# Kernel optimization log

Measured on AMD Instinct MI355X. Metric: run time of the kernel, lower is better.

## Reference

```python
import jax, jax.numpy as jnp
import numpy as np

B, S, D, H = 2, 2048, 1024, 16
DEPTH = D // H  # 64


def setup_inputs() -> dict:
    key = jax.random.key(0)
    ks = jax.random.split(key, 12)
    sc = 0.02
    q = jax.random.normal(ks[0], (B, S, D), jnp.float32)
    k = jax.random.normal(ks[1], (B, S, D), jnp.float32)
    v = jax.random.normal(ks[2], (B, S, D), jnp.float32)
    mask = jax.random.randint(ks[3], (1, 1, S, S), 0, 2, jnp.int32)
    Wq = jax.random.normal(ks[4], (D, D), jnp.float32) * sc
    bq = jnp.zeros((D,), jnp.float32)
    Wk = jax.random.normal(ks[5], (D, D), jnp.float32) * sc
    bk = jnp.zeros((D,), jnp.float32)
    Wv = jax.random.normal(ks[6], (D, DEPTH), jnp.float32) * sc
    bv = jnp.zeros((DEPTH,), jnp.float32)
    Wo = jax.random.normal(ks[7], (DEPTH, D), jnp.float32) * sc
    bo = jnp.zeros((D,), jnp.float32)
    return {"q": q, "k": k, "v": v, "mask": mask,
            "Wq": Wq, "bq": bq, "Wk": Wk, "bk": bk,
            "Wv": Wv, "bv": bv, "Wo": Wo, "bo": bo}


def reference(q, k, v, mask, Wq, bq, Wk, bk, Wv, bv, Wo, bo):
    # project and split heads: [B,S,D] -> [B,H,S,depth]
    qh = (q @ Wq + bq).reshape(B, S, H, DEPTH).transpose(0, 2, 1, 3)
    kh = (k @ Wk + bk).reshape(B, S, H, DEPTH).transpose(0, 2, 1, 3)
    vp = v @ Wv + bv  # [B,S,depth], shared across heads (no per-head split)
    scale = 1.0 / jnp.sqrt(jnp.asarray(DEPTH, jnp.float32))
    logits = jnp.einsum("bhqd,bhkd->bhqk", qh, kh) * scale
    logits = logits + mask.astype(logits.dtype) * (-1e9)
    attn = jax.nn.softmax(logits, axis=-1)  # [B,H,Sq,Sk]
    attn_mean = jnp.mean(attn, axis=1)      # [B,Sq,Sk]
    # mean over heads of (attn_h @ v) == mean(attn) @ v since V is shared
    # (dropout is identity at inference)
    ctx = jnp.einsum("bqk,bkd->bqd", attn_mean, vp)  # [B,S,depth]
    out = ctx @ Wo + bo  # [B,S,D]
    return out, attn_mean
```

## Files before the change

### kernel.cpp

```cpp
#include <hip/hip_runtime.h>
#include <hip/hip_bf16.h>

#define BB 2
#define SS 2048
#define DD 1024
#define HH 16
#define DP 64

typedef __bf16 bf16x8 __attribute__((ext_vector_type(8)));
typedef float f32x4 __attribute__((ext_vector_type(4)));

__device__ __forceinline__ unsigned short f2bf(float f) {
  unsigned u = __float_as_uint(f);
  unsigned r = u + 0x7FFFu + ((u >> 16) & 1u);
  return (unsigned short)(r >> 16);
}

__device__ __forceinline__ bf16x8 load8(const unsigned short* p) {
  return __builtin_bit_cast(bf16x8, *(const uint4*)p);
}

__device__ __forceinline__ f32x4 mfma16(bf16x8 a, bf16x8 b, f32x4 c) {
  return __builtin_amdgcn_mfma_f32_16x16x32_bf16(a, b, c, 0, 0, 0);
}

__global__ __launch_bounds__(256) void imha_prep(
    const float* __restrict__ Wq, const float* __restrict__ Wk,
    const float* __restrict__ Wo, const float* __restrict__ Wv,
    const int* __restrict__ mask,
    unsigned short* __restrict__ wqt, unsigned short* __restrict__ wkt,
    unsigned short* __restrict__ wot, unsigned short* __restrict__ wvt,
    unsigned* __restrict__ mb) {
  const int bx = blockIdx.x, t = threadIdx.x;
  if (bx < 2048) {
    const float* src = (bx < 1024) ? Wq : Wk;
    unsigned short* dst = (bx < 1024) ? wqt : wkt;
    const int tile = bx & 1023;
    const int ty = tile >> 5, tx = tile & 31;
    __shared__ float T[32][33];
    const int r = t >> 3, c4 = (t & 7) * 4;
    const float4 v = *(const float4*)&src[(ty * 32 + r) * 1024 + tx * 32 + c4];
    T[r][c4 + 0] = v.x; T[r][c4 + 1] = v.y; T[r][c4 + 2] = v.z; T[r][c4 + 3] = v.w;
    __syncthreads();
    ushort4 o;
    o.x = f2bf(T[c4 + 0][r]); o.y = f2bf(T[c4 + 1][r]);
    o.z = f2bf(T[c4 + 2][r]); o.w = f2bf(T[c4 + 3][r]);
    *(ushort4*)&dst[(tx * 32 + r) * 1024 + ty * 32 + c4] = o;
  } else if (bx < 2304) {
    const int idx = (bx - 2048) * 256 + t;
    const int n = idx >> 6, k = idx & 63;
    wot[idx] = f2bf(Wo[k * 1024 + n]);
  } else if (bx < 2816) {
    const int widx = (bx - 2304) * 256 + t;
    const int qr = widx >> 6, wd = widx & 63;
    const int* mrow = mask + qr * 2048 + wd * 32;
    unsigned wv = 0;
    #pragma unroll
    for (int j4 = 0; j4 < 8; ++j4) {
      const int4 m4 = *(const int4*)&mrow[j4 * 4];
      wv |= (unsigned)(m4.x & 1) << (j4 * 4);
      wv |= (unsigned)(m4.y & 1) << (j4 * 4 + 1);
      wv |= (unsigned)(m4.z & 1) << (j4 * 4 + 2);
      wv |= (unsigned)(m4.w & 1) << (j4 * 4 + 3);
    }
    mb[widx] = wv;
  } else {
    const int widx = (bx - 2816) * 256 + t;
    const int k = widx >> 6, n = widx & 63;
    wvt[n * 1024 + k] = f2bf(Wv[widx]);
  }
}

__global__ __launch_bounds__(256) void imha_proj(
    const float* __restrict__ X, const unsigned short* __restrict__ Wt,
    const float* __restrict__ bias, unsigned short* __restrict__ dst,
    float preScale) {
  __shared__ unsigned short As[64][40];
  __shared__ unsigned short Bs[128][40];
  const int t = threadIdx.x, l = t & 63, w = t >> 6, lr = l & 15, lg = l >> 4;
  const int m0 = blockIdx.x * 64, n0 = blockIdx.y * 128;
  const int wr = w >> 1, wc = w & 1;
  const f32x4 zf = {0.f, 0.f, 0.f, 0.f};
  f32x4 acc[2][4];
  #pragma unroll
  for (int i = 0; i < 2; ++i)
    #pragma unroll
    for (int j = 0; j < 4; ++j) acc[i][j] = zf;

  for (int kk = 0; kk < 32; ++kk) {
    {
      const int rA = t >> 2, cA = (t & 3) * 8;
      const float4 v0 = *(const float4*)&X[(m0 + rA) * 1024 + kk * 32 + cA];
      const float4 v1 = *(const float4*)&X[(m0 + rA) * 1024 + kk * 32 + cA + 4];
      ushort4 o0, o1;
      o0.x = f2bf(v0.x); o0.y = f2bf(v0.y); o0.z = f2bf(v0.z); o0.w = f2bf(v0.w);
      o1.x = f2bf(v1.x); o1.y = f2bf(v1.y); o1.z = f2bf(v1.z); o1.w = f2bf(v1.w);
      *(ushort4*)&As[rA][cA] = o0;
      *(ushort4*)&As[rA][cA + 4] = o1;
      const int rB = t >> 2, cB = (t & 3) * 8;
      #pragma unroll
      for (int p = 0; p < 2; ++p) {
        const uint4 u = *(const uint4*)&Wt[(n0 + p * 64 + rB) * 1024 + kk * 32 + cB];
        *(uint4*)&Bs[p * 64 + rB][cB] = u;
      }
    }
    __syncthreads();
    bf16x8 a[2], bf[4];
    #pragma unroll
    for (int i = 0; i < 2; ++i) a[i] = load8(&As[wr * 32 + i * 16 + lr][lg * 8]);
    #pragma unroll
    for (int j = 0; j < 4; ++j) bf[j] = load8(&Bs[wc * 64 + j * 16 + lr][lg * 8]);
    #pragma unroll
    for (int i = 0; i < 2; ++i)
      #pragma unroll
      for (int j = 0; j < 4; ++j) acc[i][j] = mfma16(a[i], bf[j], acc[i][j]);
    __syncthreads();
  }
  #pragma unroll
  for (int j = 0; j < 4; ++j) {
    const int gn = n0 + wc * 64 + j * 16 + lr;
    const float bv = bias[gn];
    const int h = gn >> 6, d = gn & 63;
    #pragma unroll
    for (int i = 0; i < 2; ++i) {
      #pragma unroll
      for (int r = 0; r < 4; ++r) {
        const int gm = m0 + wr * 32 + i * 16 + lg * 4 + r;
        const int b = gm >> 11, s = gm & 2047;
        dst[(((b * 16 + h) * 2048 + s) << 6) + d] = f2bf((acc[i][j][r] + bv) * preScale);
      }
    }
  }
}

__global__ __launch_bounds__(256) void imha_vproj_mm(
    const float* __restrict__ V, const unsigned short* __restrict__ wvt,
    float* __restrict__ ctxvp) {
  const int t = threadIdx.x, l = t & 63, w = t >> 6, lr = l & 15, lg = l >> 4;
  const int m0 = blockIdx.x * 64 + w * 16;
  const int k0 = blockIdx.y * 128;
  const f32x4 zf = {0.f, 0.f, 0.f, 0.f};
  f32x4 acc[4];
  #pragma unroll
  for (int j = 0; j < 4; ++j) acc[j] = zf;
  #pragma unroll
  for (int kk = 0; kk < 4; ++kk) {
    const int kb = k0 + kk * 32 + lg * 8;
    const float4 v0 = *(const float4*)&V[(m0 + lr) * 1024 + kb];
    const float4 v1 = *(const float4*)&V[(m0 + lr) * 1024 + kb + 4];
    union { bf16x8 v; unsigned short u[8]; } au;
    au.u[0] = f2bf(v0.x); au.u[1] = f2bf(v0.y); au.u[2] = f2bf(v0.z); au.u[3] = f2bf(v0.w);
    au.u[4] = f2bf(v1.x); au.u[5] = f2bf(v1.y); au.u[6] = f2bf(v1.z); au.u[7] = f2bf(v1.w);
    #pragma unroll
    for (int j = 0; j < 4; ++j) {
      const bf16x8 bfr = load8(&wvt[(j * 16 + lr) * 1024 + kb]);
      acc[j] = mfma16(au.v, bfr, acc[j]);
    }
  }
  #pragma unroll
  for (int j = 0; j < 4; ++j)
    #pragma unroll
    for (int reg = 0; reg < 4; ++reg) {
      const int m = m0 + lg * 4 + reg;
      ctxvp[((size_t)blockIdx.y * 4096 + m) * 64 + j * 16 + lr] = acc[j][reg];
    }
}

__global__ __launch_bounds__(256) void imha_vred(
    const float* __restrict__ ctxvp, const float* __restrict__ bv,
    unsigned short* __restrict__ vpt) {
  __shared__ float T[128][65];
  const int t = threadIdx.x;
  const int m0 = blockIdx.x * 128;
  #pragma unroll
  for (int i = 0; i < 32; ++i) {
    const int e = t + i * 256;
    float s = 0.f;
    #pragma unroll
    for (int p = 0; p < 8; ++p) s += ctxvp[(size_t)p * 262144 + (size_t)m0 * 64 + e];
    T[e >> 6][e & 63] = s;
  }
  __syncthreads();
  const int d = t >> 2, sc = (t & 3) * 32;
  const int b = m0 >> 11, srow = m0 & 2047;
  const float bias = bv[d];
  unsigned short* dst = vpt + ((size_t)b * 64 + d) * 2048 + srow + sc;
  #pragma unroll
  for (int i = 0; i < 32; i += 8) {
    ushort4 o0, o1;
    o0.x = f2bf(T[sc + i + 0][d] + bias); o0.y = f2bf(T[sc + i + 1][d] + bias);
    o0.z = f2bf(T[sc + i + 2][d] + bias); o0.w = f2bf(T[sc + i + 3][d] + bias);
    o1.x = f2bf(T[sc + i + 4][d] + bias); o1.y = f2bf(T[sc + i + 5][d] + bias);
    o1.z = f2bf(T[sc + i + 6][d] + bias); o1.w = f2bf(T[sc + i + 7][d] + bias);
    *(ushort4*)(dst + i) = o0;
    *(ushort4*)(dst + i + 4) = o1;
  }
}

__global__ __launch_bounds__(256, 3) void imha_pass1(
    const unsigned short* __restrict__ qhb, const unsigned short* __restrict__ khb,
    const unsigned* __restrict__ mb, float* __restrict__ lpart16) {
  __shared__ unsigned short Kb[2][8192];
  const int t = threadIdx.x, l = t & 63, w = t >> 6, lr = l & 15, lg = l >> 4;
  const int orig = blockIdx.x;
  const int swz = (orig & 7) * 64 + (orig >> 3);
  const int q0 = (swz & 15) * 128, bh = swz >> 4;
  const int qw = q0 + w * 32;
  const unsigned short* qb = qhb + ((size_t)(bh * 2048 + qw) << 6);
  bf16x8 aq[2][2];
  #pragma unroll
  for (int rf = 0; rf < 2; ++rf)
    #pragma unroll
    for (int k2 = 0; k2 < 2; ++k2)
      aq[rf][k2] = load8(qb + (((rf * 16 + lr) << 6) + k2 * 32 + lg * 8));
  const unsigned short* kbase = khb + ((size_t)bh << 17);
  uint4 pre[4];
  #pragma unroll
  for (int it = 0; it < 4; ++it)
    pre[it] = *(const uint4*)((const char*)kbase + (it * 256 + t) * 16);
  #pragma unroll
  for (int it = 0; it < 4; ++it) {
    const int off = (it * 256 + t) * 16, row = off >> 7, col = off & 127;
    *(uint4*)((char*)&Kb[0][0] + row * 128 + (col ^ ((row & 7) << 4))) = pre[it];
  }
  __syncthreads();
  float lsum[2][4] = {0.f, 0.f, 0.f, 0.f, 0.f, 0.f, 0.f, 0.f};
  #pragma unroll 1
  for (int kt = 0; kt < 16; ++kt) {
    if (kt < 15) {
      const char* nk = (const char*)kbase + (kt + 1) * 16384;
      #pragma unroll
      for (int it = 0; it < 4; ++it)
        pre[it] = *(const uint4*)(nk + (it * 256 + t) * 16);
    }
    uint4 mw[2][4];
    #pragma unroll
    for (int rf = 0; rf < 2; ++rf)
      #pragma unroll
      for (int reg = 0; reg < 4; ++reg) {
        const int qrow = qw + rf * 16 + lg * 4 + reg;
        mw[rf][reg] = *(const uint4*)&mb[qrow * 64 + kt * 4];
      }
    const char* kl = (const char*)&Kb[kt & 1][0];
    const int sxor = (lr & 7) << 4;
    __builtin_amdgcn_s_setprio(1);
    #pragma unroll
    for (int cf = 0; cf < 8; ++cf) {
      const int row = cf * 16 + lr;
      const bf16x8 b0 = load8((const unsigned short*)(kl + row * 128 + ((lg * 16) ^ sxor)));
      const bf16x8 b1 = load8((const unsigned short*)(kl + row * 128 + ((64 + lg * 16) ^ sxor)));
      #pragma unroll
      for (int rf = 0; rf < 2; ++rf) {
        f32x4 aini;
        #pragma unroll
        for (int reg = 0; reg < 4; ++reg) {
          const unsigned word = ((const unsigned*)&mw[rf][reg])[cf >> 1];
          const unsigned bit = (word >> (((cf & 1) << 4) + lr)) & 1u;
          aini[reg] = bit ? -30000.0f : 0.0f;
        }
        f32x4 acc = mfma16(aq[rf][0], b0, aini);
        acc = mfma16(aq[rf][1], b1, acc);
        #pragma unroll
        for (int reg = 0; reg < 4; ++reg)
          lsum[rf][reg] += __builtin_exp2f(acc[reg]);
      }
    }
    __builtin_amdgcn_s_setprio(0);
    if (kt < 15) {
      #pragma unroll
      for (int it = 0; it < 4; ++it) {
        const int off = (it * 256 + t) * 16, row = off >> 7, col = off & 127;
        *(uint4*)((char*)&Kb[(kt + 1) & 1][0] + row * 128 + (col ^ ((row & 7) << 4))) = pre[it];
      }
      __syncthreads();
    }
  }
  #pragma unroll
  for (int rf = 0; rf < 2; ++rf)
    #pragma unroll
    for (int reg = 0; reg < 4; ++reg) {
      const int qrow = bh * 2048 + qw + rf * 16 + lg * 4 + reg;
      lpart16[(qrow << 4) + lr] = lsum[rf][reg];
    }
}

__global__ __launch_bounds__(256) void imha_linv(
    const float* __restrict__ lpart16, float* __restrict__ linv) {
  const int i = blockIdx.x * 256 + threadIdx.x;
  const float4* p = (const float4*)&lpart16[i << 4];
  float s = 0.f;
  #pragma unroll
  for (int j = 0; j < 4; ++j) {
    const float4 v = p[j];
    s += v.x + v.y + v.z + v.w;
  }
  linv[i] = 0.0625f / s;
}

__global__ __launch_bounds__(256, 2) void imha_pass2(
    const unsigned short* __restrict__ qhb, const unsigned short* __restrict__ khb,
    const unsigned short* __restrict__ vpt, const unsigned* __restrict__ mb,
    const float* __restrict__ linv, float* __restrict__ attn_out,
    float* __restrict__ ctxp) {
  __shared__ unsigned short Ps[128][136];
  __shared__ unsigned short Kb[2][8192];
  const int t = threadIdx.x, l = t & 63, w = t >> 6, lr = l & 15, lg = l >> 4;
  const int orig = blockIdx.x;
  const int swz = (orig & 7) * 64 + (orig >> 3);
  const int q0 = (swz & 15) * 128, ksb = (swz >> 4) & 15, b = swz >> 8;
  const int k00 = ksb * 128;
  const int qw = q0 + w * 32;
  f32x4 aini[2][2][4];
  #pragma unroll
  for (int rf = 0; rf < 2; ++rf)
    #pragma unroll
    for (int reg = 0; reg < 4; ++reg) {
      const int qrow = qw + rf * 16 + lg * 4 + reg;
      const unsigned* mrow = mb + qrow * 64;
      #pragma unroll
      for (int kt = 0; kt < 2; ++kt)
        #pragma unroll
        for (int cf = 0; cf < 4; ++cf) {
          const unsigned word = mrow[(k00 + kt * 64 + cf * 16) >> 5];
          const unsigned bit = (word >> (((cf & 1) << 4) + lr)) & 1u;
          aini[rf][kt][cf][reg] = bit ? -30000.0f : 0.0f;
        }
    }
  float pm[2][2][4][4];
  #pragma unroll
  for (int a = 0; a < 2; ++a)
    #pragma unroll
    for (int c = 0; c < 2; ++c)
      #pragma unroll
      for (int d2 = 0; d2 < 4; ++d2)
        #pragma unroll
        for (int e = 0; e < 4; ++e) pm[a][c][d2][e] = 0.f;

  const unsigned short* kbase = khb + ((size_t)((b * 16) * 2048 + k00) << 6);
  uint4 pre[4];
  #pragma unroll
  for (int it = 0; it < 4; ++it)
    pre[it] = *(const uint4*)((const char*)kbase + (it * 256 + t) * 16);
  #pragma unroll
  for (int it = 0; it < 4; ++it) {
    const int off = (it * 256 + t) * 16, row = off >> 7, col = off & 127;
    *(uint4*)((char*)&Kb[0][0] + row * 128 + (col ^ ((row & 7) << 4))) = pre[it];
  }
  __syncthreads();
  #pragma unroll 1
  for (int h = 0; h < 16; ++h) {
    if (h < 15) {
      const char* nk = (const char*)(kbase + ((size_t)(h + 1) << 17));
      #pragma unroll
      for (int it = 0; it < 4; ++it)
        pre[it] = *(const uint4*)(nk + (it * 256 + t) * 16);
    }
    const unsigned short* qb = qhb + ((size_t)((b * 16 + h) * 2048 + qw) << 6);
    bf16x8 aq[2][2];
    #pragma unroll
    for (int rf = 0; rf < 2; ++rf)
      #pragma unroll
      for (int k2 = 0; k2 < 2; ++k2)
        aq[rf][k2] = load8(qb + (((rf * 16 + lr) << 6) + k2 * 32 + lg * 8));
    float4 li4[2];
    #pragma unroll
    for (int rf = 0; rf < 2; ++rf)
      li4[rf] = *(const float4*)&linv[(b * 16 + h) * 2048 + qw + rf * 16 + lg * 4];
    const char* kl = (const char*)&Kb[h & 1][0];
    const int sxor = (lr & 7) << 4;
    __builtin_amdgcn_s_setprio(1);
    #pragma unroll
    for (int kt = 0; kt < 2; ++kt) {
      #pragma unroll
      for (int cf = 0; cf < 4; ++cf) {
        const int row = kt * 64 + cf * 16 + lr;
        const bf16x8 b0 = load8((const unsigned short*)(kl + row * 128 + ((lg * 16) ^ sxor)));
        const bf16x8 b1 = load8((const unsigned short*)(kl + row * 128 + ((64 + lg * 16) ^ sxor)));
        #pragma unroll
        for (int rf = 0; rf < 2; ++rf) {
          f32x4 acc = mfma16(aq[rf][0], b0, aini[rf][kt][cf]);
          acc = mfma16(aq[rf][1], b1, acc);
          const float* lip = (const float*)&li4[rf];
          #pragma unroll
          for (int reg = 0; reg < 4; ++reg)
            pm[rf][kt][cf][reg] += __builtin_exp2f(acc[reg]) * lip[reg];
        }
      }
    }
    __builtin_amdgcn_s_setprio(0);
    if (h < 15) {
      #pragma unroll
      for (int it = 0; it < 4; ++it) {
        const int off = (it * 256 + t) * 16, row = off >> 7, col = off & 127;
        *(uint4*)((char*)&Kb[(h + 1) & 1][0] + row * 128 + (col ^ ((row & 7) << 4))) = pre[it];
      }
      __syncthreads();
    }
  }
  #pragma unroll
  for (int rf = 0; rf < 2; ++rf)
    #pragma unroll
    for (int kt = 0; kt < 2; ++kt)
      #pragma unroll
      for (int cf = 0; cf < 4; ++cf)
        #pragma unroll
        for (int reg = 0; reg < 4; ++reg) {
          const int qrow = qw + rf * 16 + lg * 4 + reg;
          const int col = k00 + kt * 64 + cf * 16 + lr;
          const float p = pm[rf][kt][cf][reg];
          attn_out[((size_t)(b * 2048 + qrow) << 11) + col] = p;
          Ps[w * 32 + rf * 16 + lg * 4 + reg][kt * 64 + cf * 16 + lr] = f2bf(p);
        }
  const f32x4 zf = {0.f, 0.f, 0.f, 0.f};
  f32x4 ctx[2][4];
  #pragma unroll
  for (int rf = 0; rf < 2; ++rf)
    #pragma unroll
    for (int dcf = 0; dcf < 4; ++dcf) ctx[rf][dcf] = zf;
  #pragma unroll
  for (int k2 = 0; k2 < 4; ++k2) {
    bf16x8 ap[2];
    #pragma unroll
    for (int rf = 0; rf < 2; ++rf)
      ap[rf] = load8(&Ps[w * 32 + rf * 16 + lr][k2 * 32 + lg * 8]);
    #pragma unroll
    for (int dcf = 0; dcf < 4; ++dcf) {
      const bf16x8 bvf = load8(vpt + ((size_t)(b * 64 + dcf * 16 + lr)) * 2048 + k00 + k2 * 32 + lg * 8);
      #pragma unroll
      for (int rf = 0; rf < 2; ++rf) ctx[rf][dcf] = mfma16(ap[rf], bvf, ctx[rf][dcf]);
    }
  }
  #pragma unroll
  for (int rf = 0; rf < 2; ++rf)
    #pragma unroll
    for (int dcf = 0; dcf < 4; ++dcf)
      #pragma unroll
      for (int reg = 0; reg < 4; ++reg) {
        const int m = b * 2048 + qw + rf * 16 + lg * 4 + reg;
        ctxp[((size_t)(ksb * 4096 + m) << 6) + dcf * 16 + lr] = ctx[rf][dcf][reg];
      }
}

__global__ __launch_bounds__(256) void imha_ctxred(
    const float* __restrict__ ctxp, unsigned short* __restrict__ ctxr) {
  const int i4 = (blockIdx.x * 256 + threadIdx.x) * 4;
  float4 s = {0.f, 0.f, 0.f, 0.f};
  #pragma unroll
  for (int p = 0; p < 16; ++p) {
    const float4 v = *(const float4*)&ctxp[(size_t)p * 262144 + i4];
    s.x += v.x; s.y += v.y; s.z += v.z; s.w += v.w;
  }
  ushort4 o;
  o.x = f2bf(s.x); o.y = f2bf(s.y); o.z = f2bf(s.z); o.w = f2bf(s.w);
  *(ushort4*)&ctxr[i4] = o;
}

__global__ __launch_bounds__(256) void imha_outproj(
    const unsigned short* __restrict__ ctxr, const unsigned short* __restrict__ wot,
    const float* __restrict__ bo, float* __restrict__ out) {
  __shared__ unsigned short As[128][72];
  __shared__ unsigned short Bs[128][72];
  const int t = threadIdx.x, l = t & 63, w = t >> 6, lr = l & 15, lg = l >> 4;
  const int m0 = blockIdx.x * 128, n0 = blockIdx.y * 128;
  const int wr = w >> 1, wc = w & 1;
  {
    const int r = t >> 1, cs = (t & 1) * 32;
    #pragma unroll
    for (int i = 0; i < 4; ++i)
      *(uint4*)&As[r][cs + i * 8] = *(const uint4*)&ctxr[(m0 + r) * 64 + cs + i * 8];
    #pragma unroll
    for (int i = 0; i < 4; ++i)
      *(uint4*)&Bs[r][cs + i * 8] = *(const uint4*)&wot[(n0 + r) * 64 + cs + i * 8];
  }
  __syncthreads();
  const f32x4 zf = {0.f, 0.f, 0.f, 0.f};
  f32x4 acc[4][4];
  #pragma unroll
  for (int i = 0; i < 4; ++i)
    #pragma unroll
    for (int j = 0; j < 4; ++j) acc[i][j] = zf;
  #pragma unroll
  for (int k2 = 0; k2 < 2; ++k2) {
    bf16x8 a[4], bb[4];
    #pragma unroll
    for (int i = 0; i < 4; ++i) a[i] = load8(&As[wr * 64 + i * 16 + lr][k2 * 32 + lg * 8]);
    #pragma unroll
    for (int i = 0; i < 4; ++i) bb[i] = load8(&Bs[wc * 64 + i * 16 + lr][k2 * 32 + lg * 8]);
    #pragma unroll
    for (int i = 0; i < 4; ++i)
      #pragma unroll
      for (int j = 0; j < 4; ++j) acc[i][j] = mfma16(a[i], bb[j], acc[i][j]);
  }
  #pragma unroll
  for (int j = 0; j < 4; ++j) {
    const int gn = n0 + wc * 64 + j * 16 + lr;
    const float bv = bo[gn];
    #pragma unroll
    for (int i = 0; i < 4; ++i) {
      #pragma unroll
      for (int r = 0; r < 4; ++r) {
        const int gm = m0 + wr * 64 + i * 16 + lg * 4 + r;
        out[((size_t)gm << 10) + gn] = acc[i][j][r] + bv;
      }
    }
  }
}

extern "C" void kernel_launch(void* const* d_in, const int* in_sizes, int n_in,
                              void* d_out, int out_size, void* d_ws, size_t ws_size,
                              hipStream_t stream) {
  const float* q  = (const float*)d_in[0];
  const float* k  = (const float*)d_in[1];
  const float* v  = (const float*)d_in[2];
  const int*  mask = (const int*)d_in[3];
  const float* Wq = (const float*)d_in[4];
  const float* bq = (const float*)d_in[5];
  const float* Wk = (const float*)d_in[6];
  const float* bk = (const float*)d_in[7];
  const float* Wv = (const float*)d_in[8];
  const float* bv = (const float*)d_in[9];
  const float* Wo = (const float*)d_in[10];
  const float* bo = (const float*)d_in[11];

  char* ws = (char*)d_ws;
  unsigned short* wqt  = (unsigned short*)(ws + 0);
  unsigned short* wkt  = (unsigned short*)(ws + 2097152);
  unsigned short* wot  = (unsigned short*)(ws + 4194304);
  unsigned*       mb   = (unsigned*)      (ws + 4325376);
  unsigned short* qhb  = (unsigned short*)(ws + 4849664);
  unsigned short* khb  = (unsigned short*)(ws + 13238272);
  unsigned short* vpt  = (unsigned short*)(ws + 21626880);
  float*          linv = (float*)         (ws + 22151168);
  float*          ctxp = (float*)         (ws + 22413312);
  unsigned short* ctxr = (unsigned short*)(ws + 39190528);
  unsigned short* wvt  = (unsigned short*)(ws + 22413312);
  float*          ctxvp= (float*)         (ws + 22413312 + 131072);
  float*          lpart16 = (float*)      (ws + 22413312);

  float* out  = (float*)d_out;
  float* attn = out + (size_t)BB * SS * DD;

  const float qScale = 0.125f * 1.44269504088896340736f;

  imha_prep<<<3072, 256, 0, stream>>>(Wq, Wk, Wo, Wv, mask, wqt, wkt, wot, wvt, mb);
  imha_vproj_mm<<<dim3(64, 8), 256, 0, stream>>>(v, wvt, ctxvp);
  imha_vred<<<32, 256, 0, stream>>>(ctxvp, bv, vpt);
  imha_proj<<<dim3(64, 8), 256, 0, stream>>>(q, wqt, bq, qhb, qScale);
  imha_proj<<<dim3(64, 8), 256, 0, stream>>>(k, wkt, bk, khb, 1.0f);
  imha_pass1<<<512, 256, 0, stream>>>(qhb, khb, mb, lpart16);
  imha_linv<<<256, 256, 0, stream>>>(lpart16, linv);
  imha_pass2<<<512, 256, 0, stream>>>(qhb, khb, vpt, mb, linv, attn, ctxp);
  imha_ctxred<<<256, 256, 0, stream>>>(ctxp, ctxr);
  imha_outproj<<<dim3(32, 8), 256, 0, stream>>>(ctxr, wot, bo, out);
}
```

Measured before the change: 221.0 us.

## Split pass1 over key halves and double pass2 waves per block

Pass1 now launches twice as many blocks, each covering half the keys, and writes 32 partial row sums per query that linv reduces. Pass2 uses 512 threads so each wave handles 32 queries by 64 keys instead of 32 by 128, which halves per-thread accumulator registers and splits the K-tile loads across more threads. The P·V product is repartitioned to 16 rows per wave, which needs an extra barrier before reading Ps. The aim is more parallelism and occupancy on both attention passes, at the cost of more Q and mask reloads and an extra partial-sum pass.

```diff
diff --git a/kernel.cpp b/kernel.cpp
--- a/kernel.cpp
+++ b/kernel.cpp
@@ -197,14 +197,14 @@
   }
 }
 
-__global__ __launch_bounds__(256, 3) void imha_pass1(
+__global__ __launch_bounds__(256, 4) void imha_pass1(
     const unsigned short* __restrict__ qhb, const unsigned short* __restrict__ khb,
-    const unsigned* __restrict__ mb, float* __restrict__ lpart16) {
+    const unsigned* __restrict__ mb, float* __restrict__ lpart32) {
   __shared__ unsigned short Kb[2][8192];
   const int t = threadIdx.x, l = t & 63, w = t >> 6, lr = l & 15, lg = l >> 4;
   const int orig = blockIdx.x;
-  const int swz = (orig & 7) * 64 + (orig >> 3);
-  const int q0 = (swz & 15) * 128, bh = swz >> 4;
+  const int swz = (orig & 7) * 128 + (orig >> 3);
+  const int q0 = (swz & 15) * 128, kh = (swz >> 4) & 1, bh = swz >> 5;
   const int qw = q0 + w * 32;
   const unsigned short* qb = qhb + ((size_t)(bh * 2048 + qw) << 6);
   bf16x8 aq[2][2];
@@ -213,7 +213,7 @@
     #pragma unroll
     for (int k2 = 0; k2 < 2; ++k2)
       aq[rf][k2] = load8(qb + (((rf * 16 + lr) << 6) + k2 * 32 + lg * 8));
-  const unsigned short* kbase = khb + ((size_t)bh << 17);
+  const unsigned short* kbase = khb + ((size_t)bh << 17) + ((size_t)kh << 16);
   uint4 pre[4];
   #pragma unroll
   for (int it = 0; it < 4; ++it)
@@ -226,8 +226,8 @@
   __syncthreads();
   float lsum[2][4] = {0.f, 0.f, 0.f, 0.f, 0.f, 0.f, 0.f, 0.f};
   #pragma unroll 1
-  for (int kt = 0; kt < 16; ++kt) {
-    if (kt < 15) {
+  for (int kt = 0; kt < 8; ++kt) {
+    if (kt < 7) {
       const char* nk = (const char*)kbase + (kt + 1) * 16384;
       #pragma unroll
       for (int it = 0; it < 4; ++it)
@@ -239,7 +239,7 @@
       #pragma unroll
       for (int reg = 0; reg < 4; ++reg) {
         const int qrow = qw + rf * 16 + lg * 4 + reg;
-        mw[rf][reg] = *(const uint4*)&mb[qrow * 64 + kt * 4];
+        mw[rf][reg] = *(const uint4*)&mb[qrow * 64 + kh * 32 + kt * 4];
       }
     const char* kl = (const char*)&Kb[kt & 1][0];
     const int sxor = (lr & 7) << 4;
@@ -266,7 +266,7 @@
       }
     }
     __builtin_amdgcn_s_setprio(0);
-    if (kt < 15) {
+    if (kt < 7) {
       #pragma unroll
       for (int it = 0; it < 4; ++it) {
         const int off = (it * 256 + t) * 16, row = off >> 7, col = off & 127;
@@ -280,24 +280,24 @@
     #pragma unroll
     for (int reg = 0; reg < 4; ++reg) {
       const int qrow = bh * 2048 + qw + rf * 16 + lg * 4 + reg;
-      lpart16[(qrow << 4) + lr] = lsum[rf][reg];
+      lpart32[(qrow << 5) + (kh << 4) + lr] = lsum[rf][reg];
     }
 }
 
 __global__ __launch_bounds__(256) void imha_linv(
-    const float* __restrict__ lpart16, float* __restrict__ linv) {
+    const float* __restrict__ lpart32, float* __restrict__ linv) {
   const int i = blockIdx.x * 256 + threadIdx.x;
-  const float4* p = (const float4*)&lpart16[i << 4];
+  const float4* p = (const float4*)&lpart32[i << 5];
   float s = 0.f;
   #pragma unroll
-  for (int j = 0; j < 4; ++j) {
+  for (int j = 0; j < 8; ++j) {
     const float4 v = p[j];
     s += v.x + v.y + v.z + v.w;
   }
   linv[i] = 0.0625f / s;
 }
 
-__global__ __launch_bounds__(256, 2) void imha_pass2(
+__global__ __launch_bounds__(512, 4) void imha_pass2(
     const unsigned short* __restrict__ qhb, const unsigned short* __restrict__ khb,
     const unsigned short* __restrict__ vpt, const unsigned* __restrict__ mb,
     const float* __restrict__ linv, float* __restrict__ attn_out,
@@ -305,12 +305,14 @@
   __shared__ unsigned short Ps[128][136];
   __shared__ unsigned short Kb[2][8192];
   const int t = threadIdx.x, l = t & 63, w = t >> 6, lr = l & 15, lg = l >> 4;
+  const int wq = w >> 1, wk = w & 1;
   const int orig = blockIdx.x;
   const int swz = (orig & 7) * 64 + (orig >> 3);
   const int q0 = (swz & 15) * 128, ksb = (swz >> 4) & 15, b = swz >> 8;
   const int k00 = ksb * 128;
-  const int qw = q0 + w * 32;
-  f32x4 aini[2][2][4];
+  const int qw = q0 + wq * 32;
+  const int kof = wk * 64;
+  f32x4 aini[2][4];
   #pragma unroll
   for (int rf = 0; rf < 2; ++rf)
     #pragma unroll
@@ -318,32 +320,28 @@
       const int qrow = qw + rf * 16 + lg * 4 + reg;
       const unsigned* mrow = mb + qrow * 64;
       #pragma unroll
-      for (int kt = 0; kt < 2; ++kt)
-        #pragma unroll
-        for (int cf = 0; cf < 4; ++cf) {
-          const unsigned word = mrow[(k00 + kt * 64 + cf * 16) >> 5];
-          const unsigned bit = (word >> (((cf & 1) << 4) + lr)) & 1u;
-          aini[rf][kt][cf][reg] = bit ? -30000.0f : 0.0f;
-        }
-    }
-  float pm[2][2][4][4];
+      for (int cf = 0; cf < 4; ++cf) {
+        const unsigned word = mrow[(k00 + kof + cf * 16) >> 5];
+        const unsigned bit = (word >> (((cf & 1) << 4) + lr)) & 1u;
+        aini[rf][cf][reg] = bit ? -30000.0f : 0.0f;
+      }
+    }
+  float pm[2][4][4];
   #pragma unroll
   for (int a = 0; a < 2; ++a)
     #pragma unroll
-    for (int c = 0; c < 2; ++c)
-      #pragma unroll
-      for (int d2 = 0; d2 < 4; ++d2)
-        #pragma unroll
-        for (int e = 0; e < 4; ++e) pm[a][c][d2][e] = 0.f;
+    for (int d2 = 0; d2 < 4; ++d2)
+      #pragma unroll
+      for (int e = 0; e < 4; ++e) pm[a][d2][e] = 0.f;
 
   const unsigned short* kbase = khb + ((size_t)((b * 16) * 2048 + k00) << 6);
-  uint4 pre[4];
-  #pragma unroll
-  for (int it = 0; it < 4; ++it)
-    pre[it] = *(const uint4*)((const char*)kbase + (it * 256 + t) * 16);
-  #pragma unroll
-  for (int it = 0; it < 4; ++it) {
-    const int off = (it * 256 + t) * 16, row = off >> 7, col = off & 127;
+  uint4 pre[2];
+  #pragma unroll
+  for (int it = 0; it < 2; ++it)
+    pre[it] = *(const uint4*)((const char*)kbase + (it * 512 + t) * 16);
+  #pragma unroll
+  for (int it = 0; it < 2; ++it) {
+    const int off = (it * 512 + t) * 16, row = off >> 7, col = off & 127;
     *(uint4*)((char*)&Kb[0][0] + row * 128 + (col ^ ((row & 7) << 4))) = pre[it];
   }
   __syncthreads();
@@ -352,8 +350,8 @@
     if (h < 15) {
       const char* nk = (const char*)(kbase + ((size_t)(h + 1) << 17));
       #pragma unroll
-      for (int it = 0; it < 4; ++it)
-        pre[it] = *(const uint4*)(nk + (it * 256 + t) * 16);
+      for (int it = 0; it < 2; ++it)
+        pre[it] = *(const uint4*)(nk + (it * 512 + t) * 16);
     }
     const unsigned short* qb = qhb + ((size_t)((b * 16 + h) * 2048 + qw) << 6);
     bf16x8 aq[2][2];
@@ -370,28 +368,25 @@
     const int sxor = (lr & 7) << 4;
     __builtin_amdgcn_s_setprio(1);
     #pragma unroll
-    for (int kt = 0; kt < 2; ++kt) {
-      #pragma unroll
-      for (int cf = 0; cf < 4; ++cf) {
-        const int row = kt * 64 + cf * 16 + lr;
-        const bf16x8 b0 = load8((const unsigned short*)(kl + row * 128 + ((lg * 16) ^ sxor)));
-        const bf16x8 b1 = load8((const unsigned short*)(kl + row * 128 + ((64 + lg * 16) ^ sxor)));
+    for (int cf = 0; cf < 4; ++cf) {
+      const int row = kof + cf * 16 + lr;
+      const bf16x8 b0 = load8((const unsigned short*)(kl + row * 128 + ((lg * 16) ^ sxor)));
+      const bf16x8 b1 = load8((const unsigned short*)(kl + row * 128 + ((64 + lg * 16) ^ sxor)));
+      #pragma unroll
+      for (int rf = 0; rf < 2; ++rf) {
+        f32x4 acc = mfma16(aq[rf][0], b0, aini[rf][cf]);
+        acc = mfma16(aq[rf][1], b1, acc);
+        const float* lip = (const float*)&li4[rf];
         #pragma unroll
-        for (int rf = 0; rf < 2; ++rf) {
-          f32x4 acc = mfma16(aq[rf][0], b0, aini[rf][kt][cf]);
-          acc = mfma16(aq[rf][1], b1, acc);
-          const float* lip = (const float*)&li4[rf];
-          #pragma unroll
-          for (int reg = 0; reg < 4; ++reg)
-            pm[rf][kt][cf][reg] += __builtin_exp2f(acc[reg]) * lip[reg];
-        }
+        for (int reg = 0; reg < 4; ++reg)
+          pm[rf][cf][reg] += __builtin_exp2f(acc[reg]) * lip[reg];
       }
     }
     __builtin_amdgcn_s_setprio(0);
     if (h < 15) {
       #pragma unroll
-      for (int it = 0; it < 4; ++it) {
-        const int off = (it * 256 + t) * 16, row = off >> 7, col = off & 127;
+      for (int it = 0; it < 2; ++it) {
+        const int off = (it * 512 + t) * 16, row = off >> 7, col = off & 127;
         *(uint4*)((char*)&Kb[(h + 1) & 1][0] + row * 128 + (col ^ ((row & 7) << 4))) = pre[it];
       }
       __syncthreads();
@@ -400,45 +395,36 @@
   #pragma unroll
   for (int rf = 0; rf < 2; ++rf)
     #pragma unroll
-    for (int kt = 0; kt < 2; ++kt)
-      #pragma unroll
-      for (int cf = 0; cf < 4; ++cf)
-        #pragma unroll
-        for (int reg = 0; reg < 4; ++reg) {
-          const int qrow = qw + rf * 16 + lg * 4 + reg;
-          const int col = k00 + kt * 64 + cf * 16 + lr;
-          const float p = pm[rf][kt][cf][reg];
-          attn_out[((size_t)(b * 2048 + qrow) << 11) + col] = p;
-          Ps[w * 32 + rf * 16 + lg * 4 + reg][kt * 64 + cf * 16 + lr] = f2bf(p);
-        }
+    for (int cf = 0; cf < 4; ++cf)
+      #pragma unroll
+      for (int reg = 0; reg < 4; ++reg) {
+        const int qrow = qw + rf * 16 + lg * 4 + reg;
+        const int col = k00 + kof + cf * 16 + lr;
+        const float p = pm[rf][cf][reg];
+        attn_out[((size_t)(b * 2048 + qrow) << 11) + col] = p;
+        Ps[wq * 32 + rf * 16 + lg * 4 + reg][kof + cf * 16 + lr] = f2bf(p);
+      }
+  __syncthreads();
   const f32x4 zf = {0.f, 0.f, 0.f, 0.f};
-  f32x4 ctx[2][4];
-  #pragma unroll
-  for (int rf = 0; rf < 2; ++rf)
-    #pragma unroll
-    for (int dcf = 0; dcf < 4; ++dcf) ctx[rf][dcf] = zf;
+  f32x4 ctx[4];
+  #pragma unroll
+  for (int dcf = 0; dcf < 4; ++dcf) ctx[dcf] = zf;
   #pragma unroll
   for (int k2 = 0; k2 < 4; ++k2) {
-    bf16x8 ap[2];
-    #pragma unroll
-    for (int rf = 0; rf < 2; ++rf)
-      ap[rf] = load8(&Ps[w * 32 + rf * 16 + lr][k2 * 32 + lg * 8]);
+    const bf16x8 ap = load8(&Ps[w * 16 + lr][k2 * 32 + lg * 8]);
     #pragma unroll
     for (int dcf = 0; dcf < 4; ++dcf) {
       const bf16x8 bvf = load8(vpt + ((size_t)(b * 64 + dcf * 16 + lr)) * 2048 + k00 + k2 * 32 + lg * 8);
-      #pragma unroll
-      for (int rf = 0; rf < 2; ++rf) ctx[rf][dcf] = mfma16(ap[rf], bvf, ctx[rf][dcf]);
-    }
-  }
-  #pragma unroll
-  for (int rf = 0; rf < 2; ++rf)
-    #pragma unroll
-    for (int dcf = 0; dcf < 4; ++dcf)
-      #pragma unroll
-      for (int reg = 0; reg < 4; ++reg) {
-        const int m = b * 2048 + qw + rf * 16 + lg * 4 + reg;
-        ctxp[((size_t)(ksb * 4096 + m) << 6) + dcf * 16 + lr] = ctx[rf][dcf][reg];
-      }
+      ctx[dcf] = mfma16(ap, bvf, ctx[dcf]);
+    }
+  }
+  #pragma unroll
+  for (int dcf = 0; dcf < 4; ++dcf)
+    #pragma unroll
+    for (int reg = 0; reg < 4; ++reg) {
+      const int m = b * 2048 + q0 + w * 16 + lg * 4 + reg;
+      ctxp[((size_t)(ksb * 4096 + m) << 6) + dcf * 16 + lr] = ctx[dcf][reg];
+    }
 }
 
 __global__ __launch_bounds__(256) void imha_ctxred(
@@ -535,7 +521,7 @@
   unsigned short* ctxr = (unsigned short*)(ws + 39190528);
   unsigned short* wvt  = (unsigned short*)(ws + 22413312);
   float*          ctxvp= (float*)         (ws + 22413312 + 131072);
-  float*          lpart16 = (float*)      (ws + 22413312);
+  float*          lpart32 = (float*)      (ws + 22413312);
 
   float* out  = (float*)d_out;
   float* attn = out + (size_t)BB * SS * DD;
@@ -547,9 +533,9 @@
   imha_vred<<<32, 256, 0, stream>>>(ctxvp, bv, vpt);
   imha_proj<<<dim3(64, 8), 256, 0, stream>>>(q, wqt, bq, qhb, qScale);
   imha_proj<<<dim3(64, 8), 256, 0, stream>>>(k, wkt, bk, khb, 1.0f);
-  imha_pass1<<<512, 256, 0, stream>>>(qhb, khb, mb, lpart16);
-  imha_linv<<<256, 256, 0, stream>>>(lpart16, linv);
-  imha_pass2<<<512, 256, 0, stream>>>(qhb, khb, vpt, mb, linv, attn, ctxp);
+  imha_pass1<<<1024, 256, 0, stream>>>(qhb, khb, mb, lpart32);
+  imha_linv<<<256, 256, 0, stream>>>(lpart32, linv);
+  imha_pass2<<<512, 512, 0, stream>>>(qhb, khb, vpt, mb, linv, attn, ctxp);
   imha_ctxred<<<256, 256, 0, stream>>>(ctxp, ctxr);
   imha_outproj<<<dim3(32, 8), 256, 0, stream>>>(ctxr, wot, bo, out);
 }
```

After: 258.7 us. 1.17x slower.
